# Kernel tuning notes

Hardware: AMD Instinct MI355X
Metric: run time of the kernel (lower is better)

Reference implementation:

```python
import jax, jax.numpy as jnp
import numpy as np

LN_EPS = 1e-5

def _layernorm(x, g, b):
    mu = jnp.mean(x, axis=-1, keepdims=True)
    var = jnp.var(x, axis=-1, keepdims=True)
    return (x - mu) * jax.lax.rsqrt(var + LN_EPS) * g + b

def setup_inputs() -> dict:
    key = jax.random.key(0)
    ks = jax.random.split(key, 8)
    B, T, V, H = 32, 128, 204, 128
    s = 0.02
    x = jax.random.normal(ks[0], (B, T, V, 1), dtype=jnp.float32)
    return {
        "x": x,
        # batched per-variable GRN params
        "fc1_w": jax.random.normal(ks[1], (V, H), dtype=jnp.float32) * s,
        "fc1_b": jnp.zeros((V, H), jnp.float32),
        "fc2_w": jax.random.normal(ks[2], (V, H, H), dtype=jnp.float32) * s,
        "fc2_b": jnp.zeros((V, H), jnp.float32),
        "glu_w": jax.random.normal(ks[3], (V, 2 * H, H), dtype=jnp.float32) * s,
        "glu_b": jnp.zeros((V, 2 * H), jnp.float32),
        "skip_w": jax.random.normal(ks[4], (V, H), dtype=jnp.float32) * s,
        "skip_b": jnp.zeros((V, H), jnp.float32),
        "ln_g": jnp.ones((H,), jnp.float32),
        "ln_b": jnp.zeros((H,), jnp.float32),
        # weight GRN params (input_dim=V, hidden=H, output_dim=V; identity skip)
        "wfc1_w": jax.random.normal(ks[5], (V, H), dtype=jnp.float32) * s,
        "wfc1_b": jnp.zeros((H,), jnp.float32),
        "wfc2_w": jax.random.normal(ks[6], (H, H), dtype=jnp.float32) * s,
        "wfc2_b": jnp.zeros((H,), jnp.float32),
        "wglu_w": jax.random.normal(ks[7], (H, 2 * V), dtype=jnp.float32) * s,
        "wglu_b": jnp.zeros((2 * V,), jnp.float32),
        "wln_g": jnp.ones((V,), jnp.float32),
        "wln_b": jnp.zeros((V,), jnp.float32),
    }

def reference(x, fc1_w, fc1_b, fc2_w, fc2_b, glu_w, glu_b, skip_w, skip_b, ln_g, ln_b,
              wfc1_w, wfc1_b, wfc2_w, wfc2_b, wglu_w, wglu_b, wln_g, wln_b):
    B, T, V, D = x.shape
    H = fc1_w.shape[1]
    xs = x.reshape(B * T, V)  # (N, V) since D == 1

    # --- batched per-variable GRN (eval mode: dropout is identity) ---
    h = jax.nn.elu(xs[..., None] * fc1_w + fc1_b)              # (N, V, H)
    h = jnp.einsum('nvh,vhk->nvk', h, fc2_w) + fc2_b           # bmm over V
    glu = jnp.einsum('nvh,vgh->nvg', h, glu_w) + glu_b         # (N, V, 2H)
    fc_out, gate = glu[..., :H], glu[..., H:]
    h = fc_out * jax.nn.sigmoid(gate)
    skip = xs[..., None] * skip_w + skip_b                     # (N, V, H)
    var_out = _layernorm(skip + h, ln_g, ln_b)                 # (N, V, H)

    # --- weight GRN (input_dim = output_dim = V -> identity skip) ---
    a = jax.nn.elu(xs @ wfc1_w + wfc1_b)                       # (N, H)
    a = a @ wfc2_w + wfc2_b
    g = a @ wglu_w + wglu_b                                    # (N, 2V)
    hg = g[:, :V] * jax.nn.sigmoid(g[:, V:])
    wts = jax.nn.softmax(_layernorm(xs + hg, wln_g, wln_b), axis=-1)  # (N, V)

    out = jnp.einsum('nvh,nv->nh', var_out, wts)               # (N, H)
    return out.reshape(B, T, H), wts.reshape(B, T, V)
```

## Files before the change

### kernel.cpp

```cpp
#include <hip/hip_runtime.h>
#include <hip/hip_bf16.h>

#define NROWS 4096
#define NV    204
#define NH    128
#define NG    256

#define SLOT_BYTES 32768
#define SM_OFF     (4 * SLOT_BYTES)
#define SM_BYTES   8192
#define LDS_BYTES  (SM_OFF + 2 * SM_BYTES)

typedef __bf16 bf16x8 __attribute__((ext_vector_type(8)));
typedef float  f32x4  __attribute__((ext_vector_type(4)));

__device__ __forceinline__ float elu_f(float x)  { return x > 0.f ? x : __expf(x) - 1.f; }
__device__ __forceinline__ float sigm_f(float x) { return 1.f / (1.f + __expf(-x)); }

__device__ __forceinline__ void stage16(const void* g, void* l) {
    __builtin_amdgcn_global_load_lds((const __attribute__((address_space(1))) void*)g,
                                     (__attribute__((address_space(3))) void*)l, 16, 0, 0);
}

__device__ __forceinline__ void stage_tile(const void* src, char* dst, int w, int l) {
    const char* sb = (const char*)src;
    #pragma unroll
    for (int s = 0; s < 4; ++s)
        stage16(sb + (w * 4 + s) * 1024 + l * 16, dst + (w * 4 + s) * 1024);
}

#define NB_FC2 NV
#define NB_GLU (NV * 16)
#define NB_SM  NV
#define NB_WTS (NROWS / 8)

__global__ __launch_bounds__(256) void k_setup(
    const float* __restrict__ fc2_w, __bf16* __restrict__ fc2t,
    const float* __restrict__ glu_w, __bf16* __restrict__ glu16,
    const float* __restrict__ fc1_w, const float* __restrict__ fc1_b,
    const float* __restrict__ fc2_b, const float* __restrict__ glu_b,
    const float* __restrict__ skip_w, const float* __restrict__ skip_b,
    const float* __restrict__ ln_g,  const float* __restrict__ ln_b,
    float* __restrict__ smalls,
    const float* __restrict__ xs,
    const float* __restrict__ wfc1_w, const float* __restrict__ wfc1_b,
    const float* __restrict__ wfc2_w, const float* __restrict__ wfc2_b,
    const float* __restrict__ wglu_w, const float* __restrict__ wglu_b,
    const float* __restrict__ wln_g,  const float* __restrict__ wln_b,
    float* __restrict__ wts)
{
    __shared__ float tile[64 * 129];
    __shared__ float sx[8][NV];
    __shared__ float sa[8][NH];
    __shared__ float sg[8][2 * NV];

    const int b = blockIdx.x;
    const int t = threadIdx.x;

    if (b < NB_FC2) {
        const int v = b;
        const float* s = fc2_w + (size_t)v * (NH * NH);
        __bf16*      d = fc2t + (size_t)v * (NH * NH);
        for (int h = 0; h < 2; ++h) {
            __syncthreads();
            for (int i = t; i < 64 * 32; i += 256) {
                const int k = i >> 5, n4 = (i & 31) * 4;
                const float4 f = *(const float4*)(s + (h * 64 + k) * 128 + n4);
                tile[k * 129 + n4 + 0] = f.x;
                tile[k * 129 + n4 + 1] = f.y;
                tile[k * 129 + n4 + 2] = f.z;
                tile[k * 129 + n4 + 3] = f.w;
            }
            __syncthreads();
            for (int i = t; i < 128 * 8; i += 256) {
                const int n = i >> 3, kc = (i & 7) * 8;
                bf16x8 o;
                #pragma unroll
                for (int q = 0; q < 8; ++q) o[q] = (__bf16)tile[(kc + q) * 129 + n];
                const int ch  = h * 8 + (i & 7);
                const int chs = ch ^ (n & 7);
                *(bf16x8*)(d + n * 128 + chs * 8) = o;
            }
        }
        return;
    }

    if (b < NB_FC2 + NB_GLU) {
        const int idx = (b - NB_FC2) * 256 + t;
        const int ch = idx & 15;
        const int g  = (idx >> 4) & 255;
        const int v  = idx >> 12;
        const float* sp = glu_w + (((size_t)v * NG + g) * NH + ch * 8);
        bf16x8 o;
        #pragma unroll
        for (int q = 0; q < 8; ++q) o[q] = (__bf16)sp[q];
        const int dch = ch ^ (g & 7);
        *(bf16x8*)(glu16 + (((size_t)v * NG + g) * NH) + dch * 8) = o;
        return;
    }

    if (b < NB_FC2 + NB_GLU + NB_SM) {
        const int v = b - (NB_FC2 + NB_GLU);
        float* dst = smalls + (size_t)v * 2048;
        for (int idx = t; idx < 1152; idx += 256) {
            float val;
            if      (idx < 128)  val = fc1_w[v * NH + idx];
            else if (idx < 256)  val = fc1_b[v * NH + idx - 128];
            else if (idx < 384)  val = fc2_b[v * NH + idx - 256];
            else if (idx < 640)  val = glu_b[v * NG + idx - 384];
            else if (idx < 768)  val = skip_w[v * NH + idx - 640];
            else if (idx < 896)  val = skip_b[v * NH + idx - 768];
            else if (idx < 1024) val = ln_g[idx - 896];
            else                 val = ln_b[idx - 1024];
            dst[idx] = val;
        }
        return;
    }

    const int r0 = (b - NB_FC2 - NB_GLU - NB_SM) * 8;
    const int tr = t >> 5;
    const int tc = t & 31;

    for (int i = t; i < 8 * NV; i += 256) {
        const int r = i / NV, c = i - r * NV;
        sx[r][c] = xs[(size_t)(r0 + r) * NV + c];
    }
    __syncthreads();

    float acc1[4];
    #pragma unroll
    for (int j = 0; j < 4; ++j) acc1[j] = wfc1_b[tc + 32 * j];
    for (int v = 0; v < NV; ++v) {
        const float xv = sx[tr][v];
        #pragma unroll
        for (int j = 0; j < 4; ++j)
            acc1[j] = fmaf(xv, wfc1_w[v * NH + tc + 32 * j], acc1[j]);
    }
    #pragma unroll
    for (int j = 0; j < 4; ++j) sa[tr][tc + 32 * j] = elu_f(acc1[j]);
    __syncthreads();

    float acc2[4];
    #pragma unroll
    for (int j = 0; j < 4; ++j) acc2[j] = wfc2_b[tc + 32 * j];
    for (int h = 0; h < NH; ++h) {
        const float av = sa[tr][h];
        #pragma unroll
        for (int j = 0; j < 4; ++j)
            acc2[j] = fmaf(av, wfc2_w[h * NH + tc + 32 * j], acc2[j]);
    }
    __syncthreads();
    #pragma unroll
    for (int j = 0; j < 4; ++j) sa[tr][tc + 32 * j] = acc2[j];
    __syncthreads();

    float accg[13];
    #pragma unroll
    for (int gi = 0; gi < 12; ++gi) accg[gi] = wglu_b[tc + 32 * gi];
    accg[12] = (tc < 24) ? wglu_b[tc + 384] : 0.f;
    for (int h = 0; h < NH; ++h) {
        const float av = sa[tr][h];
        #pragma unroll
        for (int gi = 0; gi < 12; ++gi)
            accg[gi] = fmaf(av, wglu_w[h * (2 * NV) + tc + 32 * gi], accg[gi]);
        if (tc < 24) accg[12] = fmaf(av, wglu_w[h * (2 * NV) + tc + 384], accg[12]);
    }
    __syncthreads();
    #pragma unroll
    for (int gi = 0; gi < 12; ++gi) sg[tr][tc + 32 * gi] = accg[gi];
    if (tc < 24) sg[tr][tc + 384] = accg[12];
    __syncthreads();

    float tv[7];
    float s1 = 0.f, s2 = 0.f;
    #pragma unroll
    for (int ii = 0; ii < 7; ++ii) {
        const int c = tc + 32 * ii;
        float val = 0.f;
        if (c < NV) {
            const float hg = sg[tr][c] * sigm_f(sg[tr][c + NV]);
            val = sx[tr][c] + hg;
            s1 += val; s2 = fmaf(val, val, s2);
        }
        tv[ii] = val;
    }
    #pragma unroll
    for (int m = 1; m <= 16; m <<= 1) { s1 += __shfl_xor(s1, m); s2 += __shfl_xor(s2, m); }
    const float mu  = s1 * (1.f / 204.f);
    const float var = s2 * (1.f / 204.f) - mu * mu;
    const float rs  = rsqrtf(fmaxf(var, 0.f) + 1e-5f);

    float mx = -1e30f;
    #pragma unroll
    for (int ii = 0; ii < 7; ++ii) {
        const int c = tc + 32 * ii;
        if (c < NV) {
            const float y = fmaf((tv[ii] - mu) * rs, wln_g[c], wln_b[c]);
            tv[ii] = y;
            mx = fmaxf(mx, y);
        }
    }
    #pragma unroll
    for (int m = 1; m <= 16; m <<= 1) mx = fmaxf(mx, __shfl_xor(mx, m));
    float se = 0.f;
    #pragma unroll
    for (int ii = 0; ii < 7; ++ii) {
        const int c = tc + 32 * ii;
        if (c < NV) {
            const float e = __expf(tv[ii] - mx);
            tv[ii] = e;
            se += e;
        }
    }
    #pragma unroll
    for (int m = 1; m <= 16; m <<= 1) se += __shfl_xor(se, m);
    const float inv = 1.f / se;
    #pragma unroll
    for (int ii = 0; ii < 7; ++ii) {
        const int c = tc + 32 * ii;
        if (c < NV) wts[(size_t)(r0 + tr) * NV + c] = tv[ii] * inv;
    }
}

__global__ __launch_bounds__(512, 2) void k_main(
    const float*  __restrict__ xs,
    const __bf16* __restrict__ fc2t,
    const __bf16* __restrict__ glu16,
    const float*  __restrict__ smalls,
    const float*  __restrict__ wts,
    float*        __restrict__ out)
{
    __shared__ __align__(16) char lds[LDS_BYTES];

    const int tid = threadIdx.x;
    const int w   = tid >> 6;
    const int l   = tid & 63;
    const int l15 = l & 15;
    const int lg  = l >> 4;
    const int sw7 = l15 & 7;

    const int vg = blockIdx.x & 7;
    const int m0 = (blockIdx.x >> 3) * 128 + w * 16;
    const int nv = (NV - 1 - vg) / 8 + 1;
    const size_t rowoff = (size_t)(m0 + l15) * NV;

    const f32x4 zero4 = {0.f, 0.f, 0.f, 0.f};
    f32x4 acc_out[8];
    #pragma unroll
    for (int j = 0; j < 8; ++j) acc_out[j] = zero4;

    const int  sh0 = l15 + ((lg & 1) << 5);
    const int  sh1 = sh0 + 16;
    const bool rlo = (lg < 2);

    float xv, wv, xn, wn;
    {
        const int v = vg;
        stage_tile(fc2t + (size_t)v * (NH * NH), lds + 0 * SLOT_BYTES, w, l);
        stage16((const char*)(smalls + (size_t)v * 2048) + w * 1024 + l * 16,
                lds + SM_OFF + w * 1024);
        xv = xs[rowoff + v];
        wv = wts[rowoff + v];
        const __bf16* g0 = glu16 + (size_t)v * (NG * NH);
        stage_tile(g0,            lds + 1 * SLOT_BYTES, w, l);
        stage_tile(g0 + 128 * NH, lds + 2 * SLOT_BYTES, w, l);
    }

    for (int i = 0; i < nv; ++i) {
        const int v     = vg + 8 * i;
        const int vnext = (i + 1 < nv) ? v + 8 : v;
        const int s0 = (3 * i) & 3, s1 = (3 * i + 1) & 3, s2 = (3 * i + 2) & 3;
        const float* sm = (const float*)(lds + SM_OFF + (i & 1) * SM_BYTES);

        asm volatile("s_waitcnt vmcnt(8)" ::: "memory");
        __builtin_amdgcn_s_barrier();
        stage_tile(fc2t + (size_t)vnext * (NH * NH), lds + ((3 * i + 3) & 3) * SLOT_BYTES, w, l);
        stage16((const char*)(smalls + (size_t)vnext * 2048) + w * 1024 + l * 16,
                lds + SM_OFF + ((i + 1) & 1) * SM_BYTES + w * 1024);
        xn = xs[rowoff + vnext];
        wn = wts[rowoff + vnext];

        bf16x8 a1[4];
        #pragma unroll
        for (int kb = 0; kb < 4; ++kb) {
            const int k0 = kb * 32 + lg * 8;
            const float4 w0 = *(const float4*)(sm + k0);
            const float4 w1 = *(const float4*)(sm + k0 + 4);
            const float4 b0 = *(const float4*)(sm + 128 + k0);
            const float4 b1 = *(const float4*)(sm + 128 + k0 + 4);
            bf16x8 af;
            af[0] = (__bf16)elu_f(fmaf(xv, w0.x, b0.x));
            af[1] = (__bf16)elu_f(fmaf(xv, w0.y, b0.y));
            af[2] = (__bf16)elu_f(fmaf(xv, w0.z, b0.z));
            af[3] = (__bf16)elu_f(fmaf(xv, w0.w, b0.w));
            af[4] = (__bf16)elu_f(fmaf(xv, w1.x, b1.x));
            af[5] = (__bf16)elu_f(fmaf(xv, w1.y, b1.y));
            af[6] = (__bf16)elu_f(fmaf(xv, w1.z, b1.z));
            af[7] = (__bf16)elu_f(fmaf(xv, w1.w, b1.w));
            a1[kb] = af;
        }

        f32x4 h2f[8];
        {
            const char* slotA = lds + s0 * SLOT_BYTES;
            #pragma unroll
            for (int j = 0; j < 8; ++j) {
                f32x4 acc = zero4;
                const char* rp = slotA + (j * 16 + l15) * 256;
                #pragma unroll
                for (int kb = 0; kb < 4; ++kb) {
                    const bf16x8 wf = *(const bf16x8*)(rp + (((kb * 4 + lg) ^ sw7) << 4));
                    acc = __builtin_amdgcn_mfma_f32_16x16x32_bf16(wf, a1[kb], acc, 0, 0, 0);
                }
                const float4 fb = *(const float4*)(sm + 256 + j * 16 + lg * 4);
                acc[0] += fb.x; acc[1] += fb.y; acc[2] += fb.z; acc[3] += fb.w;
                h2f[j] = acc;
            }
        }

        bf16x8 b2[4];
        #pragma unroll
        for (int kb2 = 0; kb2 < 4; ++kb2) {
            union U { __bf16 h[4]; int i2[2]; };
            U P, Q;
            P.h[0] = (__bf16)h2f[2 * kb2 + 0][0]; P.h[1] = (__bf16)h2f[2 * kb2 + 0][1];
            P.h[2] = (__bf16)h2f[2 * kb2 + 0][2]; P.h[3] = (__bf16)h2f[2 * kb2 + 0][3];
            Q.h[0] = (__bf16)h2f[2 * kb2 + 1][0]; Q.h[1] = (__bf16)h2f[2 * kb2 + 1][1];
            Q.h[2] = (__bf16)h2f[2 * kb2 + 1][2]; Q.h[3] = (__bf16)h2f[2 * kb2 + 1][3];
            const int px0 = __shfl(P.i2[0], sh0), qx0 = __shfl(Q.i2[0], sh0);
            const int py0 = __shfl(P.i2[1], sh0), qy0 = __shfl(Q.i2[1], sh0);
            const int px1 = __shfl(P.i2[0], sh1), qx1 = __shfl(Q.i2[0], sh1);
            const int py1 = __shfl(P.i2[1], sh1), qy1 = __shfl(Q.i2[1], sh1);
            union V { int i[4]; bf16x8 v; } R;
            R.i[0] = rlo ? px0 : qx0;
            R.i[1] = rlo ? py0 : qy0;
            R.i[2] = rlo ? px1 : qx1;
            R.i[3] = rlo ? py1 : qy1;
            b2[kb2] = R.v;
        }

        asm volatile("s_waitcnt vmcnt(11)" ::: "memory");
        __builtin_amdgcn_s_barrier();
        const __bf16* gn = glu16 + (size_t)vnext * (NG * NH);
        stage_tile(gn, lds + ((3 * i + 4) & 3) * SLOT_BYTES, w, l);

        f32x4 fco[8];
        {
            const char* slotF = lds + s1 * SLOT_BYTES;
            #pragma unroll
            for (int j = 0; j < 8; ++j) {
                f32x4 acc = zero4;
                const char* rp = slotF + (j * 16 + l15) * 256;
                #pragma unroll
                for (int kb = 0; kb < 4; ++kb) {
                    const bf16x8 wf = *(const bf16x8*)(rp + (((kb * 4 + lg) ^ sw7) << 4));
                    acc = __builtin_amdgcn_mfma_f32_16x16x32_bf16(wf, b2[kb], acc, 0, 0, 0);
                }
                const float4 gb = *(const float4*)(sm + 384 + j * 16 + lg * 4);
                acc[0] += gb.x; acc[1] += gb.y; acc[2] += gb.z; acc[3] += gb.w;
                fco[j] = acc;
            }
        }

        asm volatile("s_waitcnt vmcnt(11)" ::: "memory");
        __builtin_amdgcn_s_barrier();
        stage_tile(gn + 128 * NH, lds + ((3 * i + 5) & 3) * SLOT_BYTES, w, l);

        f32x4 sv[8];
        {
            const char* slotG = lds + s2 * SLOT_BYTES;
            #pragma unroll
            for (int j = 0; j < 8; ++j) {
                f32x4 ag = zero4;
                const char* rp = slotG + (j * 16 + l15) * 256;
                #pragma unroll
                for (int kb = 0; kb < 4; ++kb) {
                    const bf16x8 wg = *(const bf16x8*)(rp + (((kb * 4 + lg) ^ sw7) << 4));
                    ag = __builtin_amdgcn_mfma_f32_16x16x32_bf16(wg, b2[kb], ag, 0, 0, 0);
                }
                const float4 bga = *(const float4*)(sm + 512 + j * 16 + lg * 4);
                const float4 sw4 = *(const float4*)(sm + 640 + j * 16 + lg * 4);
                const float4 sb4 = *(const float4*)(sm + 768 + j * 16 + lg * 4);
                f32x4 s;
                s[0] = fmaf(xv, sw4.x, sb4.x) + fco[j][0] * sigm_f(ag[0] + bga.x);
                s[1] = fmaf(xv, sw4.y, sb4.y) + fco[j][1] * sigm_f(ag[1] + bga.y);
                s[2] = fmaf(xv, sw4.z, sb4.z) + fco[j][2] * sigm_f(ag[2] + bga.z);
                s[3] = fmaf(xv, sw4.w, sb4.w) + fco[j][3] * sigm_f(ag[3] + bga.w);
                sv[j] = s;
            }
        }

        float t1 = 0.f, t2 = 0.f;
        #pragma unroll
        for (int j = 0; j < 8; ++j) {
            #pragma unroll
            for (int r = 0; r < 4; ++r) { t1 += sv[j][r]; t2 = fmaf(sv[j][r], sv[j][r], t2); }
        }
        t1 += __shfl_xor(t1, 16); t2 += __shfl_xor(t2, 16);
        t1 += __shfl_xor(t1, 32); t2 += __shfl_xor(t2, 32);
        const float mu  = t1 * (1.f / 128.f);
        const float var = t2 * (1.f / 128.f) - mu * mu;
        const float rsv = rsqrtf(fmaxf(var, 0.f) + 1e-5f);

        #pragma unroll
        for (int j = 0; j < 8; ++j) {
            const float4 lg4 = *(const float4*)(sm + 896  + j * 16 + lg * 4);
            const float4 lb4 = *(const float4*)(sm + 1024 + j * 16 + lg * 4);
            const float y0 = fmaf((sv[j][0] - mu) * rsv, lg4.x, lb4.x);
            const float y1 = fmaf((sv[j][1] - mu) * rsv, lg4.y, lb4.y);
            const float y2 = fmaf((sv[j][2] - mu) * rsv, lg4.z, lb4.z);
            const float y3 = fmaf((sv[j][3] - mu) * rsv, lg4.w, lb4.w);
            acc_out[j][0] = fmaf(wv, y0, acc_out[j][0]);
            acc_out[j][1] = fmaf(wv, y1, acc_out[j][1]);
            acc_out[j][2] = fmaf(wv, y2, acc_out[j][2]);
            acc_out[j][3] = fmaf(wv, y3, acc_out[j][3]);
        }

        xv = xn; wv = wn;
    }

    asm volatile("s_waitcnt vmcnt(0)" ::: "memory");

    #pragma unroll
    for (int j = 0; j < 8; ++j) {
        #pragma unroll
        for (int r = 0; r < 4; ++r)
            atomicAdd(&out[(size_t)(m0 + l15) * NH + j * 16 + lg * 4 + r], acc_out[j][r]);
    }
}

extern "C" void kernel_launch(void* const* d_in, const int* in_sizes, int n_in,
                              void* d_out, int out_size, void* d_ws, size_t ws_size,
                              hipStream_t stream) {
    (void)in_sizes; (void)n_in; (void)out_size; (void)ws_size;

    const float* xs     = (const float*)d_in[0];
    const float* fc1_w  = (const float*)d_in[1];
    const float* fc1_b  = (const float*)d_in[2];
    const float* fc2_w  = (const float*)d_in[3];
    const float* fc2_b  = (const float*)d_in[4];
    const float* glu_w  = (const float*)d_in[5];
    const float* glu_b  = (const float*)d_in[6];
    const float* skip_w = (const float*)d_in[7];
    const float* skip_b = (const float*)d_in[8];
    const float* ln_g   = (const float*)d_in[9];
    const float* ln_b   = (const float*)d_in[10];
    const float* wfc1_w = (const float*)d_in[11];
    const float* wfc1_b = (const float*)d_in[12];
    const float* wfc2_w = (const float*)d_in[13];
    const float* wfc2_b = (const float*)d_in[14];
    const float* wglu_w = (const float*)d_in[15];
    const float* wglu_b = (const float*)d_in[16];
    const float* wln_g  = (const float*)d_in[17];
    const float* wln_b  = (const float*)d_in[18];

    float* out = (float*)d_out;
    float* wts = out + (size_t)NROWS * NH;

    __bf16* fc2t   = (__bf16*)d_ws;
    __bf16* glu16  = fc2t + (size_t)NV * NH * NH;
    float*  smalls = (float*)(glu16 + (size_t)NV * NG * NH);

    hipMemsetAsync(d_out, 0, (size_t)NROWS * NH * sizeof(float), stream);

    k_setup<<<NB_FC2 + NB_GLU + NB_SM + NB_WTS, 256, 0, stream>>>(
        fc2_w, fc2t, glu_w, glu16,
        fc1_w, fc1_b, fc2_b, glu_b, skip_w, skip_b, ln_g, ln_b, smalls,
        xs, wfc1_w, wfc1_b, wfc2_w, wfc2_b, wglu_w, wglu_b, wln_g, wln_b, wts);

    k_main<<<(NROWS / 128) * 8, 512, 0, stream>>>(xs, fc2t, glu16, smalls, wts, out);
}
```

Measured before the change: 384.5 us.

## Shrink k_main blocks and double-buffer weight halves to cut LDS and raise occupancy

k_main moves from 512-thread blocks with a four-slot 32KB weight ring to 256-thread blocks over 64 rows and 16 variable groups. Each 128x128 bf16 weight tile is now streamed as two 16KB halves, alternating between two LDS buffers with a __syncthreads before each refill, and the LayerNorm gamma/beta are staged once rather than per variable. Less LDS per block is meant to let more blocks reside per CU and hide latency through occupancy. In exchange the weights are re-read from L2 for twice as many row blocks, there are many more full-block barriers, and the prefetch distance is shorter.

```diff
diff --git a/kernel.cpp b/kernel.cpp
--- a/kernel.cpp
+++ b/kernel.cpp
@@ -6,10 +6,11 @@
 #define NH    128
 #define NG    256
 
-#define SLOT_BYTES 32768
-#define SM_OFF     (4 * SLOT_BYTES)
-#define SM_BYTES   8192
-#define LDS_BYTES  (SM_OFF + 2 * SM_BYTES)
+#define HALF_BYTES 16384
+#define SMS_OFF    (2 * HALF_BYTES)
+#define SMS_BYTES  3584
+#define LN_OFF     (SMS_OFF + 2 * SMS_BYTES)
+#define LDS_BYTES  (LN_OFF + 1024)
 
 typedef __bf16 bf16x8 __attribute__((ext_vector_type(8)));
 typedef float  f32x4  __attribute__((ext_vector_type(4)));
@@ -22,11 +23,16 @@
                                      (__attribute__((address_space(3))) void*)l, 16, 0, 0);
 }
 
-__device__ __forceinline__ void stage_tile(const void* src, char* dst, int w, int l) {
+__device__ __forceinline__ void stage_half(const void* src, char* dst, int w, int l) {
     const char* sb = (const char*)src;
     #pragma unroll
     for (int s = 0; s < 4; ++s)
         stage16(sb + (w * 4 + s) * 1024 + l * 16, dst + (w * 4 + s) * 1024);
+}
+
+__device__ __forceinline__ void stage_smalls(const float* src, char* dst, int w, int l) {
+    if (w < 3)       stage16((const char*)src + w * 1024 + l * 16, dst + w * 1024);
+    else if (l < 32) stage16((const char*)src + 3072 + l * 16,     dst + 3072);
 }
 
 #define NB_FC2 NV
@@ -40,7 +46,6 @@
     const float* __restrict__ fc1_w, const float* __restrict__ fc1_b,
     const float* __restrict__ fc2_b, const float* __restrict__ glu_b,
     const float* __restrict__ skip_w, const float* __restrict__ skip_b,
-    const float* __restrict__ ln_g,  const float* __restrict__ ln_b,
     float* __restrict__ smalls,
     const float* __restrict__ xs,
     const float* __restrict__ wfc1_w, const float* __restrict__ wfc1_b,
@@ -102,16 +107,14 @@
     if (b < NB_FC2 + NB_GLU + NB_SM) {
         const int v = b - (NB_FC2 + NB_GLU);
         float* dst = smalls + (size_t)v * 2048;
-        for (int idx = t; idx < 1152; idx += 256) {
+        for (int idx = t; idx < 896; idx += 256) {
             float val;
             if      (idx < 128)  val = fc1_w[v * NH + idx];
             else if (idx < 256)  val = fc1_b[v * NH + idx - 128];
             else if (idx < 384)  val = fc2_b[v * NH + idx - 256];
             else if (idx < 640)  val = glu_b[v * NG + idx - 384];
             else if (idx < 768)  val = skip_w[v * NH + idx - 640];
-            else if (idx < 896)  val = skip_b[v * NH + idx - 768];
-            else if (idx < 1024) val = ln_g[idx - 896];
-            else                 val = ln_b[idx - 1024];
+            else                 val = skip_b[v * NH + idx - 768];
             dst[idx] = val;
         }
         return;
@@ -222,11 +225,13 @@
     }
 }
 
-__global__ __launch_bounds__(512, 2) void k_main(
+__global__ __launch_bounds__(256, 4) void k_main(
     const float*  __restrict__ xs,
     const __bf16* __restrict__ fc2t,
     const __bf16* __restrict__ glu16,
     const float*  __restrict__ smalls,
+    const float*  __restrict__ ln_g,
+    const float*  __restrict__ ln_b,
     const float*  __restrict__ wts,
     float*        __restrict__ out)
 {
@@ -239,9 +244,9 @@
     const int lg  = l >> 4;
     const int sw7 = l15 & 7;
 
-    const int vg = blockIdx.x & 7;
-    const int m0 = (blockIdx.x >> 3) * 128 + w * 16;
-    const int nv = (NV - 1 - vg) / 8 + 1;
+    const int vg = blockIdx.x & 15;
+    const int m0 = (blockIdx.x >> 4) * 64 + w * 16;
+    const int nv = (NV - 1 - vg) / 16 + 1;
     const size_t rowoff = (size_t)(m0 + l15) * NV;
 
     const f32x4 zero4 = {0.f, 0.f, 0.f, 0.f};
@@ -253,32 +258,29 @@
     const int  sh1 = sh0 + 16;
     const bool rlo = (lg < 2);
 
+    const float* lnS = (const float*)(lds + LN_OFF);
+
     float xv, wv, xn, wn;
     {
-        const int v = vg;
-        stage_tile(fc2t + (size_t)v * (NH * NH), lds + 0 * SLOT_BYTES, w, l);
-        stage16((const char*)(smalls + (size_t)v * 2048) + w * 1024 + l * 16,
-                lds + SM_OFF + w * 1024);
-        xv = xs[rowoff + v];
-        wv = wts[rowoff + v];
-        const __bf16* g0 = glu16 + (size_t)v * (NG * NH);
-        stage_tile(g0,            lds + 1 * SLOT_BYTES, w, l);
-        stage_tile(g0 + 128 * NH, lds + 2 * SLOT_BYTES, w, l);
+        stage_half(fc2t + (size_t)vg * (NH * NH), lds, w, l);
+        stage_smalls(smalls + (size_t)vg * 2048, lds + SMS_OFF, w, l);
+        if (w == 0) {
+            const char* p = (l < 32) ? ((const char*)ln_g + l * 16)
+                                     : ((const char*)ln_b + (l - 32) * 16);
+            stage16(p, lds + LN_OFF);
+        }
+        xv = xs[rowoff + vg];
+        wv = wts[rowoff + vg];
     }
 
     for (int i = 0; i < nv; ++i) {
-        const int v     = vg + 8 * i;
-        const int vnext = (i + 1 < nv) ? v + 8 : v;
-        const int s0 = (3 * i) & 3, s1 = (3 * i + 1) & 3, s2 = (3 * i + 2) & 3;
-        const float* sm = (const float*)(lds + SM_OFF + (i & 1) * SM_BYTES);
-
-        asm volatile("s_waitcnt vmcnt(8)" ::: "memory");
-        __builtin_amdgcn_s_barrier();
-        stage_tile(fc2t + (size_t)vnext * (NH * NH), lds + ((3 * i + 3) & 3) * SLOT_BYTES, w, l);
-        stage16((const char*)(smalls + (size_t)vnext * 2048) + w * 1024 + l * 16,
-                lds + SM_OFF + ((i + 1) & 1) * SM_BYTES + w * 1024);
-        xn = xs[rowoff + vnext];
-        wn = wts[rowoff + vnext];
+        const int v  = vg + 16 * i;
+        const int vn = (i + 1 < nv) ? v + 16 : v;
+        const float* sm = (const float*)(lds + SMS_OFF + (i & 1) * SMS_BYTES);
+        const __bf16* gluv = glu16 + (size_t)v * (NG * NH);
+
+        __syncthreads();
+        stage_half(fc2t + (size_t)v * (NH * NH) + 64 * NH, lds + HALF_BYTES, w, l);
 
         bf16x8 a1[4];
         #pragma unroll
@@ -301,21 +303,35 @@
         }
 
         f32x4 h2f[8];
-        {
-            const char* slotA = lds + s0 * SLOT_BYTES;
-            #pragma unroll
-            for (int j = 0; j < 8; ++j) {
-                f32x4 acc = zero4;
-                const char* rp = slotA + (j * 16 + l15) * 256;
-                #pragma unroll
-                for (int kb = 0; kb < 4; ++kb) {
-                    const bf16x8 wf = *(const bf16x8*)(rp + (((kb * 4 + lg) ^ sw7) << 4));
-                    acc = __builtin_amdgcn_mfma_f32_16x16x32_bf16(wf, a1[kb], acc, 0, 0, 0);
-                }
-                const float4 fb = *(const float4*)(sm + 256 + j * 16 + lg * 4);
-                acc[0] += fb.x; acc[1] += fb.y; acc[2] += fb.z; acc[3] += fb.w;
-                h2f[j] = acc;
-            }
+        #pragma unroll
+        for (int j = 0; j < 4; ++j) {
+            f32x4 acc = zero4;
+            const char* rp = lds + (j * 16 + l15) * 256;
+            #pragma unroll
+            for (int kb = 0; kb < 4; ++kb) {
+                const bf16x8 wf = *(const bf16x8*)(rp + (((kb * 4 + lg) ^ sw7) << 4));
+                acc = __builtin_amdgcn_mfma_f32_16x16x32_bf16(wf, a1[kb], acc, 0, 0, 0);
+            }
+            const float4 fb = *(const float4*)(sm + 256 + j * 16 + lg * 4);
+            acc[0] += fb.x; acc[1] += fb.y; acc[2] += fb.z; acc[3] += fb.w;
+            h2f[j] = acc;
+        }
+
+        __syncthreads();
+        stage_half(gluv, lds, w, l);
+
+        #pragma unroll
+        for (int j = 4; j < 8; ++j) {
+            f32x4 acc = zero4;
+            const char* rp = lds + HALF_BYTES + ((j - 4) * 16 + l15) * 256;
+            #pragma unroll
+            for (int kb = 0; kb < 4; ++kb) {
+                const bf16x8 wf = *(const bf16x8*)(rp + (((kb * 4 + lg) ^ sw7) << 4));
+                acc = __builtin_amdgcn_mfma_f32_16x16x32_bf16(wf, a1[kb], acc, 0, 0, 0);
+            }
+            const float4 fb = *(const float4*)(sm + 256 + j * 16 + lg * 4);
+            acc[0] += fb.x; acc[1] += fb.y; acc[2] += fb.z; acc[3] += fb.w;
+            h2f[j] = acc;
         }
 
         bf16x8 b2[4];
@@ -331,63 +347,98 @@
             const int py0 = __shfl(P.i2[1], sh0), qy0 = __shfl(Q.i2[1], sh0);
             const int px1 = __shfl(P.i2[0], sh1), qx1 = __shfl(Q.i2[0], sh1);
             const int py1 = __shfl(P.i2[1], sh1), qy1 = __shfl(Q.i2[1], sh1);
-            union V { int i[4]; bf16x8 v; } R;
-            R.i[0] = rlo ? px0 : qx0;
-            R.i[1] = rlo ? py0 : qy0;
-            R.i[2] = rlo ? px1 : qx1;
-            R.i[3] = rlo ? py1 : qy1;
-            b2[kb2] = R.v;
-        }
-
-        asm volatile("s_waitcnt vmcnt(11)" ::: "memory");
-        __builtin_amdgcn_s_barrier();
-        const __bf16* gn = glu16 + (size_t)vnext * (NG * NH);
-        stage_tile(gn, lds + ((3 * i + 4) & 3) * SLOT_BYTES, w, l);
+            union V { int ii[4]; bf16x8 vv; } R;
+            R.ii[0] = rlo ? px0 : qx0;
+            R.ii[1] = rlo ? py0 : qy0;
+            R.ii[2] = rlo ? px1 : qx1;
+            R.ii[3] = rlo ? py1 : qy1;
+            b2[kb2] = R.vv;
+        }
+
+        __syncthreads();
+        stage_half(gluv + 64 * NH, lds + HALF_BYTES, w, l);
 
         f32x4 fco[8];
-        {
-            const char* slotF = lds + s1 * SLOT_BYTES;
-            #pragma unroll
-            for (int j = 0; j < 8; ++j) {
-                f32x4 acc = zero4;
-                const char* rp = slotF + (j * 16 + l15) * 256;
-                #pragma unroll
-                for (int kb = 0; kb < 4; ++kb) {
-                    const bf16x8 wf = *(const bf16x8*)(rp + (((kb * 4 + lg) ^ sw7) << 4));
-                    acc = __builtin_amdgcn_mfma_f32_16x16x32_bf16(wf, b2[kb], acc, 0, 0, 0);
-                }
-                const float4 gb = *(const float4*)(sm + 384 + j * 16 + lg * 4);
-                acc[0] += gb.x; acc[1] += gb.y; acc[2] += gb.z; acc[3] += gb.w;
-                fco[j] = acc;
-            }
-        }
-
-        asm volatile("s_waitcnt vmcnt(11)" ::: "memory");
-        __builtin_amdgcn_s_barrier();
-        stage_tile(gn + 128 * NH, lds + ((3 * i + 5) & 3) * SLOT_BYTES, w, l);
+        #pragma unroll
+        for (int j = 0; j < 4; ++j) {
+            f32x4 acc = zero4;
+            const char* rp = lds + (j * 16 + l15) * 256;
+            #pragma unroll
+            for (int kb = 0; kb < 4; ++kb) {
+                const bf16x8 wf = *(const bf16x8*)(rp + (((kb * 4 + lg) ^ sw7) << 4));
+                acc = __builtin_amdgcn_mfma_f32_16x16x32_bf16(wf, b2[kb], acc, 0, 0, 0);
+            }
+            const float4 gb = *(const float4*)(sm + 384 + j * 16 + lg * 4);
+            acc[0] += gb.x; acc[1] += gb.y; acc[2] += gb.z; acc[3] += gb.w;
+            fco[j] = acc;
+        }
+
+        __syncthreads();
+        stage_half(gluv + 128 * NH, lds, w, l);
+
+        #pragma unroll
+        for (int j = 4; j < 8; ++j) {
+            f32x4 acc = zero4;
+            const char* rp = lds + HALF_BYTES + ((j - 4) * 16 + l15) * 256;
+            #pragma unroll
+            for (int kb = 0; kb < 4; ++kb) {
+                const bf16x8 wf = *(const bf16x8*)(rp + (((kb * 4 + lg) ^ sw7) << 4));
+                acc = __builtin_amdgcn_mfma_f32_16x16x32_bf16(wf, b2[kb], acc, 0, 0, 0);
+            }
+            const float4 gb = *(const float4*)(sm + 384 + j * 16 + lg * 4);
+            acc[0] += gb.x; acc[1] += gb.y; acc[2] += gb.z; acc[3] += gb.w;
+            fco[j] = acc;
+        }
+
+        __syncthreads();
+        stage_half(gluv + 192 * NH, lds + HALF_BYTES, w, l);
 
         f32x4 sv[8];
-        {
-            const char* slotG = lds + s2 * SLOT_BYTES;
-            #pragma unroll
-            for (int j = 0; j < 8; ++j) {
-                f32x4 ag = zero4;
-                const char* rp = slotG + (j * 16 + l15) * 256;
-                #pragma unroll
-                for (int kb = 0; kb < 4; ++kb) {
-                    const bf16x8 wg = *(const bf16x8*)(rp + (((kb * 4 + lg) ^ sw7) << 4));
-                    ag = __builtin_amdgcn_mfma_f32_16x16x32_bf16(wg, b2[kb], ag, 0, 0, 0);
-                }
-                const float4 bga = *(const float4*)(sm + 512 + j * 16 + lg * 4);
-                const float4 sw4 = *(const float4*)(sm + 640 + j * 16 + lg * 4);
-                const float4 sb4 = *(const float4*)(sm + 768 + j * 16 + lg * 4);
-                f32x4 s;
-                s[0] = fmaf(xv, sw4.x, sb4.x) + fco[j][0] * sigm_f(ag[0] + bga.x);
-                s[1] = fmaf(xv, sw4.y, sb4.y) + fco[j][1] * sigm_f(ag[1] + bga.y);
-                s[2] = fmaf(xv, sw4.z, sb4.z) + fco[j][2] * sigm_f(ag[2] + bga.z);
-                s[3] = fmaf(xv, sw4.w, sb4.w) + fco[j][3] * sigm_f(ag[3] + bga.w);
-                sv[j] = s;
-            }
+        #pragma unroll
+        for (int j = 0; j < 4; ++j) {
+            f32x4 acc = zero4;
+            const char* rp = lds + (j * 16 + l15) * 256;
+            #pragma unroll
+            for (int kb = 0; kb < 4; ++kb) {
+                const bf16x8 wg = *(const bf16x8*)(rp + (((kb * 4 + lg) ^ sw7) << 4));
+                acc = __builtin_amdgcn_mfma_f32_16x16x32_bf16(wg, b2[kb], acc, 0, 0, 0);
+            }
+            const float4 bga = *(const float4*)(sm + 512 + j * 16 + lg * 4);
+            const float4 sw4 = *(const float4*)(sm + 640 + j * 16 + lg * 4);
+            const float4 sb4 = *(const float4*)(sm + 768 + j * 16 + lg * 4);
+            f32x4 s;
+            s[0] = fmaf(xv, sw4.x, sb4.x) + fco[j][0] * sigm_f(acc[0] + bga.x);
+            s[1] = fmaf(xv, sw4.y, sb4.y) + fco[j][1] * sigm_f(acc[1] + bga.y);
+            s[2] = fmaf(xv, sw4.z, sb4.z) + fco[j][2] * sigm_f(acc[2] + bga.z);
+            s[3] = fmaf(xv, sw4.w, sb4.w) + fco[j][3] * sigm_f(acc[3] + bga.w);
+            sv[j] = s;
+        }
+
+        __syncthreads();
+        stage_half(fc2t + (size_t)vn * (NH * NH), lds, w, l);
+        stage_smalls(smalls + (size_t)vn * 2048,
+                     lds + SMS_OFF + ((i + 1) & 1) * SMS_BYTES, w, l);
+        xn = xs[rowoff + vn];
+        wn = wts[rowoff + vn];
+
+        #pragma unroll
+        for (int j = 4; j < 8; ++j) {
+            f32x4 acc = zero4;
+            const char* rp = lds + HALF_BYTES + ((j - 4) * 16 + l15) * 256;
+            #pragma unroll
+            for (int kb = 0; kb < 4; ++kb) {
+                const bf16x8 wg = *(const bf16x8*)(rp + (((kb * 4 + lg) ^ sw7) << 4));
+                acc = __builtin_amdgcn_mfma_f32_16x16x32_bf16(wg, b2[kb], acc, 0, 0, 0);
+            }
+            const float4 bga = *(const float4*)(sm + 512 + j * 16 + lg * 4);
+            const float4 sw4 = *(const float4*)(sm + 640 + j * 16 + lg * 4);
+            const float4 sb4 = *(const float4*)(sm + 768 + j * 16 + lg * 4);
+            f32x4 s;
+            s[0] = fmaf(xv, sw4.x, sb4.x) + fco[j][0] * sigm_f(acc[0] + bga.x);
+            s[1] = fmaf(xv, sw4.y, sb4.y) + fco[j][1] * sigm_f(acc[1] + bga.y);
+            s[2] = fmaf(xv, sw4.z, sb4.z) + fco[j][2] * sigm_f(acc[2] + bga.z);
+            s[3] = fmaf(xv, sw4.w, sb4.w) + fco[j][3] * sigm_f(acc[3] + bga.w);
+            sv[j] = s;
         }
 
         float t1 = 0.f, t2 = 0.f;
@@ -404,8 +455,8 @@
 
         #pragma unroll
         for (int j = 0; j < 8; ++j) {
-            const float4 lg4 = *(const float4*)(sm + 896  + j * 16 + lg * 4);
-            const float4 lb4 = *(const float4*)(sm + 1024 + j * 16 + lg * 4);
+            const float4 lg4 = *(const float4*)(lnS + j * 16 + lg * 4);
+            const float4 lb4 = *(const float4*)(lnS + 128 + j * 16 + lg * 4);
             const float y0 = fmaf((sv[j][0] - mu) * rsv, lg4.x, lb4.x);
             const float y1 = fmaf((sv[j][1] - mu) * rsv, lg4.y, lb4.y);
             const float y2 = fmaf((sv[j][2] - mu) * rsv, lg4.z, lb4.z);
@@ -465,8 +516,9 @@
 
     k_setup<<<NB_FC2 + NB_GLU + NB_SM + NB_WTS, 256, 0, stream>>>(
         fc2_w, fc2t, glu_w, glu16,
-        fc1_w, fc1_b, fc2_b, glu_b, skip_w, skip_b, ln_g, ln_b, smalls,
+        fc1_w, fc1_b, fc2_b, glu_b, skip_w, skip_b, smalls,
         xs, wfc1_w, wfc1_b, wfc2_w, wfc2_b, wglu_w, wglu_b, wln_g, wln_b, wts);
 
-    k_main<<<(NROWS / 128) * 8, 512, 0, stream>>>(xs, fc2t, glu16, smalls, wts, out);
+    k_main<<<(NROWS / 64) * 16, 256, 0, stream>>>(xs, fc2t, glu16, smalls,
+                                                  ln_g, ln_b, wts, out);
 }
```

Measured after the change: 520.5 us. 35.4% more time.
